# Performance work log

Measured on AMD Instinct MI355X. Metric: run time of the kernel, lower is better.

The kernel has to match this reference:

```python
import jax, jax.numpy as jnp
from jax import lax
import numpy as np

V, E, NF = 50000, 300, 1          # vocab, embed_size, n_features
H = 256                            # hidden size (both layers)
B, TH, TB = 128, 32, 512           # batch, headline len, body len
NC = 4                             # n_classes


def setup_inputs() -> dict:
    key = jax.random.key(0)
    ks = jax.random.split(key, 24)
    emb = jax.random.normal(ks[0], (V, E), jnp.float32) * 0.1
    emb = emb.at[0].set(0.0)  # pad token -> zero row so seqlen masking is meaningful

    def make_ids(kid, klen, T):
        raw = jax.random.randint(kid, (B, T, NF), 1, V)
        lens = jax.random.randint(klen, (B,), max(T // 4, 1), T + 1)
        mask = jnp.arange(T)[None, :, None] < lens[:, None, None]
        return jnp.where(mask, raw, 0)

    headline_ids = make_ids(ks[1], ks[2], TH)
    body_ids = make_ids(ks[3], ks[4], TB)

    def gru_params(k, din, h):
        k1, k2 = jax.random.split(k, 2)
        s = 1.0 / np.sqrt(din + h)
        return (jax.random.normal(k1, (din + h, 2 * h), jnp.float32) * s,
                jnp.ones((2 * h,), jnp.float32),          # TF GRUCell gate bias init = 1.0
                jax.random.normal(k2, (din + h, h), jnp.float32) * s,
                jnp.zeros((h,), jnp.float32))

    D0 = NF * E
    hd0 = gru_params(ks[5], D0, H)
    hd1 = gru_params(ks[6], H, H)
    bd0 = gru_params(ks[7], D0, H)
    bd1 = gru_params(ks[8], H, H)

    W_pred = jax.random.normal(ks[9], (2 * H, NC), jnp.float32) * (1.0 / np.sqrt(2 * H))
    b_pred = jnp.zeros((NC,), jnp.float32)

    out = {"headline_ids": headline_ids, "body_ids": body_ids, "embeddings": emb,
           "W_pred": W_pred, "b_pred": b_pred}
    for pref, p in (("hd0", hd0), ("hd1", hd1), ("bd0", bd0), ("bd1", bd1)):
        out[pref + "_Wg"], out[pref + "_bg"], out[pref + "_Wc"], out[pref + "_bc"] = p
    return out


def _seq_length(x):
    # used = sign(max(|x|, axis=2)); seqlen = sum over time
    return jnp.sum(jnp.sign(jnp.max(jnp.abs(x), axis=2)), axis=1).astype(jnp.int32)


def _gru_layer(x, seqlen, Wg, bg, Wc, bc):
    # x: [B, T, D] -> outputs [B, T, H], final state [B, H]; dynamic_rnn semantics:
    # past seqlen, output is zero and state is copied through.
    Bsz, T, _ = x.shape
    Hh = Wc.shape[1]
    xt = jnp.swapaxes(x, 0, 1)  # [T, B, D]
    tids = jnp.arange(T)

    def step(h, inp):
        xi, t = inp
        xh = jnp.concatenate([xi, h], axis=-1)
        r, u = jnp.split(jax.nn.sigmoid(xh @ Wg + bg), 2, axis=-1)
        c = jnp.tanh(jnp.concatenate([xi, r * h], axis=-1) @ Wc + bc)
        nh = u * h + (1.0 - u) * c
        valid = (t < seqlen)[:, None]
        out = jnp.where(valid, nh, 0.0)
        h_next = jnp.where(valid, nh, h)
        return h_next, out

    h0 = jnp.zeros((Bsz, Hh), x.dtype)
    hf, outs = lax.scan(step, h0, (xt, tids))
    return jnp.swapaxes(outs, 0, 1), hf


def _stream(ids, emb, layers):
    x = emb[ids].reshape(ids.shape[0], ids.shape[1], -1)  # [B, T, NF*E]
    h = None
    for (Wg, bg, Wc, bc) in layers:
        sl = _seq_length(x)  # recomputed from current layer inputs, as in the source
        x, h = _gru_layer(x, sl, Wg, bg, Wc, bc)
    return h


def reference(headline_ids, body_ids, embeddings,
              hd0_Wg, hd0_bg, hd0_Wc, hd0_bc, hd1_Wg, hd1_bg, hd1_Wc, hd1_bc,
              bd0_Wg, bd0_bg, bd0_Wc, bd0_bc, bd1_Wg, bd1_bg, bd1_Wc, bd1_bc,
              W_pred, b_pred):
    h_head = _stream(headline_ids, embeddings,
                     [(hd0_Wg, hd0_bg, hd0_Wc, hd0_bc), (hd1_Wg, hd1_bg, hd1_Wc, hd1_bc)])
    h_body = _stream(body_ids, embeddings,
                     [(bd0_Wg, bd0_bg, bd0_Wc, bd0_bc), (bd1_Wg, bd1_bg, bd1_Wc, bd1_bc)])
    pred_input = jnp.concatenate([h_head, h_body], axis=1)  # [B, 2H]
    return pred_input @ W_pred + b_pred                      # [B, NC]
```

## Files before the change

### kernel.cpp

```cpp
#include <hip/hip_runtime.h>
#include <cstdint>
#include <cstddef>

#define H_    256
#define NG    768
#define BATCH 128
#define TH_   32
#define TB_   512
#define E_    300
#define RPB   16
#define NBLK  (BATCH / RPB)

typedef _Float16 half8 __attribute__((ext_vector_type(8)));
typedef _Float16 half4 __attribute__((ext_vector_type(4)));
typedef float    floatx4 __attribute__((ext_vector_type(4)));

#define AS1 __attribute__((address_space(1)))
#define AS3 __attribute__((address_space(3)))

#define WC_LGKM0 0xC07F
#define WCVM(N)  (0x0F70 | ((N) & 15) | (((N) >> 4) << 14))

__global__ __launch_bounds__(256) void pack_bias(
    const float* __restrict__ bg, const float* __restrict__ bc,
    float* __restrict__ bias)
{
  int idx = blockIdx.x * 256 + threadIdx.x;
  if (idx < NG) bias[idx] = (idx < 2 * H_) ? bg[idx] : bc[idx - 2 * H_];
}

__global__ __launch_bounds__(256) void pack_bx(
    const float* __restrict__ Wg, const float* __restrict__ Wc,
    int din, int KT, _Float16* __restrict__ out)
{
  int idx = blockIdx.x * 256 + threadIdx.x;
  if (idx >= KT * 48 * 64) return;
  int lane = idx & 63, tile = idx >> 6;
  int kt = tile / 48, nt = tile - kt * 48;
  int col = nt * 16 + (lane & 15);
  int k0 = kt * 32 + (lane >> 4) * 8;
  const float* W; int ncols, c2;
  if (col < 2 * H_) { W = Wg; ncols = 2 * H_; c2 = col; }
  else              { W = Wc; ncols = H_;     c2 = col - 2 * H_; }
  _Float16* dst = out + ((size_t)(kt * 48 + nt) * 64 + lane) * 8;
#pragma unroll
  for (int j = 0; j < 8; ++j) {
    int k = k0 + j;
    dst[j] = (k < din) ? (_Float16)W[(size_t)k * ncols + c2] : (_Float16)0.f;
  }
}

__global__ __launch_bounds__(256) void pack_w(
    const float* __restrict__ Wg, const float* __restrict__ Wc, int din,
    _Float16* __restrict__ wpk)
{
  int idx = blockIdx.x * 256 + threadIdx.x;
  if (idx >= 48 * 64) return;
  int tile = idx >> 6, lane = idx & 63;
  int grp = tile >> 4, tt = tile & 15;
  int wv = tt >> 1, s = tt & 1;
  const float* W; int ncols, n0;
  if (grp == 0)      { W = Wg; ncols = 2 * H_; n0 = wv * 32 + s * 16; }
  else if (grp == 1) { W = Wg; ncols = 2 * H_; n0 = 256 + wv * 32 + s * 16; }
  else               { W = Wc; ncols = H_;     n0 = wv * 32 + s * 16; }
  int n = n0 + (lane & 15);
  int kb = (lane >> 4) * 8;
#pragma unroll
  for (int kt = 0; kt < 8; ++kt) {
    _Float16* dst = wpk + ((size_t)(tile * 8 + kt) * 64 + lane) * 8;
#pragma unroll
    for (int j = 0; j < 8; ++j)
      dst[j] = (_Float16)W[(size_t)(din + kt * 32 + kb + j) * ncols + n];
  }
}

__global__ __launch_bounds__(256) void seq_k(const int* __restrict__ ids, int T,
                                             int* __restrict__ seq)
{
  __shared__ int red[256];
  int b = blockIdx.x, tid = threadIdx.x;
  int cnt = 0;
  for (int t = tid; t < T; t += 256) cnt += (ids[b * T + t] != 0) ? 1 : 0;
  red[tid] = cnt;
  __syncthreads();
  for (int s = 128; s > 0; s >>= 1) {
    if (tid < s) red[tid] += red[tid + s];
    __syncthreads();
  }
  if (tid == 0) seq[b] = red[0];
}

struct GruJob {
  const _Float16* G; const _Float16* W; const int* seq;
  _Float16* outp; float* state; int t0; int tc;
};
struct GemmJob {
  const _Float16* Adir; const int* ids; const _Float16* Bpk;
  const float* bias; _Float16* G;
  int K; int KT; int t0; int tcsh; int T;
};
struct StageArgs {
  GruJob  gj[4];
  GemmJob mj[4];
  const float* emb;
  int ngru; int ngemm;
  int goff[4];
};

union SMem {
  struct { _Float16 hpk[4096]; _Float16 rpk[4096]; _Float16 Gs[4][12288]; } g;
  struct { _Float16 Al[2][64 * 40]; _Float16 Bl[2][8 * 512]; } m;
};

__device__ __forceinline__ void gemm_block(const GemmJob& jb, const float* emb,
                                           int lb, SMem& sm)
{
  auto& Al = sm.m.Al;
  auto& Bl = sm.m.Bl;
  const int tid = threadIdx.x;
  const int w = tid >> 6, lane = tid & 63;
  const int quad = lane >> 4, l15 = lane & 15;
  const int gx = lb / 6, gy = lb - gx * 6;
  const int m0 = gx * 64, n0 = gy * 128;
  const int K = jb.K, KT = jb.KT, tcsh = jb.tcsh;
  const int tc = 1 << tcsh;

  const int am = tid >> 3, ak = tid & 7;
  const int arow = m0 + am;
  const _Float16* asrch = nullptr;
  const float*    asrcf = nullptr;
  if (jb.Adir) {
    asrch = jb.Adir + (size_t)arow * K;
  } else {
    int b = arow >> tcsh, tl = arow & (tc - 1);
    asrcf = emb + (size_t)jb.ids[b * jb.T + jb.t0 + tl] * K;
  }

  float a4[4];
  auto loadA = [&](int kt) {
    int k0 = kt * 32 + ak * 4;
    if (asrch) {
      half4 hv = *(const half4*)&asrch[k0];
#pragma unroll
      for (int j = 0; j < 4; ++j) a4[j] = (float)hv[j];
    } else {
#pragma unroll
      for (int j = 0; j < 4; ++j) a4[j] = (k0 + j < K) ? asrcf[k0 + j] : 0.f;
    }
  };
  auto writeA = [&](int buf) {
    half4 v;
#pragma unroll
    for (int j = 0; j < 4; ++j) v[j] = (_Float16)a4[j];
    *(half4*)&Al[buf][am * 40 + ak * 4] = v;
  };
  auto stageB = [&](int kt, int buf) {
    int nt = (n0 >> 4) + w;
    const _Float16* src = jb.Bpk + ((size_t)(kt * 48 + nt) * 64 + lane) * 8;
    __builtin_amdgcn_global_load_lds(
        (const AS1 unsigned int*)src,
        (AS3 unsigned int*)&Bl[buf][w * 512 + lane * 8], 16, 0, 0);
  };

  loadA(0);
  stageB(0, 0);
  writeA(0);
  floatx4 acc[4] = {};

  for (int kt = 0; kt < KT; ++kt) {
    const int buf = kt & 1;
    __syncthreads();
    if (kt + 1 < KT) { loadA(kt + 1); stageB(kt + 1, buf ^ 1); }
    half8 bf = *(const half8*)&Bl[buf][w * 512 + lane * 8];
#pragma unroll
    for (int st = 0; st < 4; ++st) {
      half8 af = *(const half8*)&Al[buf][(st * 16 + l15) * 40 + quad * 8];
      acc[st] = __builtin_amdgcn_mfma_f32_16x16x32_f16(af, bf, acc[st], 0, 0, 0);
    }
    if (kt + 1 < KT) writeA(buf ^ 1);
  }

  int col = n0 + w * 16 + l15;
  float bb = jb.bias[col];
  int g = col >> 8, kk = col & 255;
  int ww = kk >> 5, ss = (kk >> 4) & 1, ll = kk & 15;
  int cc = 2 * g + ss;
#pragma unroll
  for (int st = 0; st < 4; ++st) {
#pragma unroll
    for (int r = 0; r < 4; ++r) {
      int grow = m0 + st * 16 + quad * 4 + r;
      int b = grow >> tcsh, tl = grow & (tc - 1);
      int rg = b >> 4, mm = b & 15, qb = mm >> 2, rb = mm & 3;
      jb.G[((size_t)tl * BATCH + rg * RPB) * NG +
           ((ww * 6 + cc) * 64 + qb * 16 + ll) * 4 + rb] =
          (_Float16)(acc[st][r] + bb);
    }
  }
}

__device__ __forceinline__ void gru_block(const GruJob& jb, int rg, SMem& sm)
{
  _Float16* hpk = sm.g.hpk;
  _Float16* rpk = sm.g.rpk;
  auto& Gs = sm.g.Gs;

  const _Float16* G = jb.G;
  if (!G) return;
  const _Float16* Wsrc = jb.W;
  _Float16* outp = jb.outp;
  float* state = jb.state;
  const int t0 = jb.t0, tc = jb.tc;

  const int tid = threadIdx.x;
  const int w = tid >> 6, lane = tid & 63;
  const int quad = lane >> 4, l15 = lane & 15;

  floatx4 wg[4][8];
  floatx4 wc[2][8];
#pragma unroll
  for (int i = 0; i < 4; ++i) {
    const int tile = (i >> 1) * 16 + w * 2 + (i & 1);
#pragma unroll
    for (int kt = 0; kt < 8; ++kt) {
      wg[i][kt] = *(const floatx4*)&Wsrc[((size_t)(tile * 8 + kt) * 64 + lane) * 8];
      asm volatile("" : "+v"(wg[i][kt]));
    }
  }
#pragma unroll
  for (int i = 0; i < 2; ++i) {
    const int tile = 32 + w * 2 + i;
#pragma unroll
    for (int kt = 0; kt < 8; ++kt) {
      wc[i][kt] = *(const floatx4*)&Wsrc[((size_t)(tile * 8 + kt) * 64 + lane) * 8];
      asm volatile("" : "+a"(wc[i][kt]));
    }
  }

  int seq4[4];
#pragma unroll
  for (int r = 0; r < 4; ++r) seq4[r] = jb.seq[rg * RPB + quad * 4 + r];
  int Smax = 0;
#pragma unroll
  for (int i = 0; i < 16; ++i) Smax = max(Smax, jb.seq[rg * RPB + i]);
  int steps = Smax - t0;
  if (steps < 0) steps = 0;
  if (steps > tc) steps = tc;

  const int wbase = (w * 64 + quad * 2 + (l15 >> 3)) * 8 + (l15 & 7);
  const int rbase = (((quad >> 1) << 5) + ((l15 & 3) << 3) +
                     ((l15 >> 2) << 1) + (quad & 1)) * 8;

  float h_reg[2][4];
#pragma unroll
  for (int s = 0; s < 2; ++s)
#pragma unroll
    for (int r = 0; r < 4; ++r) {
      int row = quad * 4 + r, k = w * 32 + s * 16 + l15;
      float v = (t0 == 0) ? 0.f : state[(size_t)(rg * RPB + row) * H_ + k];
      h_reg[s][r] = v;
      hpk[wbase + s * 256 + r * 64] = (_Float16)v;
    }

  const _Float16* gblk = G + (size_t)rg * RPB * NG + w * 1536;
  _Float16* ldsw = &Gs[0][0] + w * 1536;
  auto stage = [&](int t, int buf) {
    const _Float16* gp = gblk + (size_t)t * BATCH * NG;
    _Float16* lp = ldsw + buf * 12288;
#pragma unroll
    for (int i = 0; i < 3; ++i) {
      __builtin_amdgcn_global_load_lds(
          (const AS1 unsigned int*)(gp + i * 512 + lane * 8),
          (AS3 unsigned int*)(lp + i * 512), 16, 0, 0);
    }
  };
  if (steps > 0) stage(0, 0);
  __syncthreads();
  if (steps > 1) stage(1, 1);
  if (steps > 2) stage(2, 2);

  const _Float16* hA = &hpk[rbase];
  const _Float16* rA = &rpk[rbase];

  __builtin_amdgcn_s_setprio(1);
  for (int t = 0; t < steps; ++t) {
    const int buf = t & 3;
    if (t + 3 < steps) stage(t + 3, (t + 3) & 3);

    floatx4 acc[4] = {};
#pragma unroll
    for (int kt = 0; kt < 8; ++kt) {
      half8 a = *(const half8*)&hA[kt * 512];
#pragma unroll
      for (int s = 0; s < 4; ++s)
        acc[s] = __builtin_amdgcn_mfma_f32_16x16x32_f16(
            a, __builtin_bit_cast(half8, wg[s][kt]), acc[s], 0, 0, 0);
    }

    {
      int np = outp ? ((t < 3) ? t : 3) : 0;
      int nf = steps - 1 - t; if (nf > 3) nf = 3;
      switch (np * 4 + nf) {
        case  0: __builtin_amdgcn_s_waitcnt(WCVM(0));  break;
        case  1: __builtin_amdgcn_s_waitcnt(WCVM(3));  break;
        case  2: __builtin_amdgcn_s_waitcnt(WCVM(6));  break;
        case  3: __builtin_amdgcn_s_waitcnt(WCVM(9));  break;
        case  4: __builtin_amdgcn_s_waitcnt(WCVM(8));  break;
        case  5: __builtin_amdgcn_s_waitcnt(WCVM(11)); break;
        case  6: __builtin_amdgcn_s_waitcnt(WCVM(14)); break;
        case  7: __builtin_amdgcn_s_waitcnt(WCVM(17)); break;
        case  8: __builtin_amdgcn_s_waitcnt(WCVM(16)); break;
        case  9: __builtin_amdgcn_s_waitcnt(WCVM(19)); break;
        case 10: __builtin_amdgcn_s_waitcnt(WCVM(22)); break;
        case 11: __builtin_amdgcn_s_waitcnt(WCVM(25)); break;
        case 12: __builtin_amdgcn_s_waitcnt(WCVM(24)); break;
        case 13: __builtin_amdgcn_s_waitcnt(WCVM(27)); break;
        case 14: __builtin_amdgcn_s_waitcnt(WCVM(30)); break;
        default: __builtin_amdgcn_s_waitcnt(WCVM(33)); break;
      }
    }

    floatx4 gA[4];
#pragma unroll
    for (int c = 0; c < 4; ++c) {
      half4 hv = *(const half4*)&Gs[buf][(w * 6 + c) * 256 + lane * 4];
#pragma unroll
      for (int j = 0; j < 4; ++j) gA[c][j] = (float)hv[j];
    }

#pragma unroll
    for (int s = 0; s < 2; ++s)
#pragma unroll
      for (int r = 0; r < 4; ++r) {
        float pre = acc[s][r] + gA[s][r];
        float g = __builtin_amdgcn_rcpf(1.f + __expf(-pre));
        rpk[wbase + s * 256 + r * 64] = (_Float16)(g * h_reg[s][r]);
      }
    float u_reg[2][4];
#pragma unroll
    for (int s = 0; s < 2; ++s)
#pragma unroll
      for (int r = 0; r < 4; ++r) {
        float pre = acc[2 + s][r] + gA[2 + s][r];
        u_reg[s][r] = __builtin_amdgcn_rcpf(1.f + __expf(-pre));
      }
    __builtin_amdgcn_s_waitcnt(WC_LGKM0);
    __builtin_amdgcn_s_barrier();

    floatx4 accB[2] = {};
#pragma unroll
    for (int kt = 0; kt < 8; ++kt) {
      half8 a = *(const half8*)&rA[kt * 512];
#pragma unroll
      for (int s = 0; s < 2; ++s)
        accB[s] = __builtin_amdgcn_mfma_f32_16x16x32_f16(
            a, __builtin_bit_cast(half8, wc[s][kt]), accB[s], 0, 0, 0);
    }
    floatx4 gB[2];
#pragma unroll
    for (int s = 0; s < 2; ++s) {
      half4 hv = *(const half4*)&Gs[buf][(w * 6 + 4 + s) * 256 + lane * 4];
#pragma unroll
      for (int j = 0; j < 4; ++j) gB[s][j] = (float)hv[j];
    }

#pragma unroll
    for (int s = 0; s < 2; ++s)
#pragma unroll
      for (int r = 0; r < 4; ++r) {
        int row = quad * 4 + r;
        float pre = accB[s][r] + gB[s][r];
        float c = 1.f - 2.f * __builtin_amdgcn_rcpf(1.f + __expf(2.f * pre));
        float u = u_reg[s][r];
        float hn = u * h_reg[s][r] + (1.f - u) * c;
        bool valid = (t0 + t) < seq4[r];
        hn = valid ? hn : h_reg[s][r];
        h_reg[s][r] = hn;
        hpk[wbase + s * 256 + r * 64] = (_Float16)hn;
        if (outp)
          outp[((size_t)(rg * RPB + row) * tc + t) * H_ + (w * 32 + s * 16 + l15)] =
              (_Float16)(valid ? hn : 0.f);
      }
    __builtin_amdgcn_s_waitcnt(WC_LGKM0);
    __builtin_amdgcn_s_barrier();
  }
  __builtin_amdgcn_s_setprio(0);
#pragma unroll
  for (int s = 0; s < 2; ++s)
#pragma unroll
    for (int r = 0; r < 4; ++r)
      state[(size_t)(rg * RPB + quad * 4 + r) * H_ + (w * 32 + s * 16 + l15)] =
          h_reg[s][r];
}

__global__ __launch_bounds__(512, 1) void mega(StageArgs a)
{
  __shared__ SMem sm;
  const int bid = blockIdx.x;
  const int ngrub = a.ngru * NBLK;
  if (bid < ngrub) {
    gru_block(a.gj[bid >> 3], bid & 7, sm);
  } else {
    int lb = bid - ngrub;
    int j = 0;
#pragma unroll
    for (int k = 1; k < 4; ++k)
      if (k < a.ngemm && lb >= a.goff[k]) j = k;
    gemm_block(a.mj[j], a.emb, lb - a.goff[j], sm);
  }
}

__global__ __launch_bounds__(512) void pred_k(
    const float* __restrict__ hh, const float* __restrict__ hb,
    const float* __restrict__ Wp, const float* __restrict__ bpred,
    float* __restrict__ out)
{
  int tid = threadIdx.x;
  int b = tid >> 2, c = tid & 3;
  float acc = bpred[c];
  for (int k = 0; k < H_; ++k) acc += hh[b * H_ + k] * Wp[k * 4 + c];
  for (int k = 0; k < H_; ++k) acc += hb[b * H_ + k] * Wp[(H_ + k) * 4 + c];
  out[b * 4 + c] = acc;
}

extern "C" void kernel_launch(void* const* d_in, const int* in_sizes, int n_in,
                              void* d_out, int out_size, void* d_ws, size_t ws_size,
                              hipStream_t stream)
{
  (void)in_sizes; (void)n_in; (void)out_size;
  const int*   idsH = (const int*)  d_in[0];
  const int*   idsB = (const int*)  d_in[1];
  const float* emb  = (const float*)d_in[2];
  const float* Wp   = (const float*)d_in[3];
  const float* bp   = (const float*)d_in[4];
  const float* W[4][4];
  for (int s = 0; s < 4; ++s)
    for (int q = 0; q < 4; ++q)
      W[s][q] = (const float*)d_in[5 + s * 4 + q];

  float* wbase = (float*)d_ws;
  size_t off = 0;
  auto alloc = [&](size_t n) {
    float* p = wbase + off; off += (n + 255) & ~(size_t)255; return p;
  };
  int* seqH = (int*)alloc(BATCH);
  int* seqB = (int*)alloc(BATCH);
  float* bi[4]; _Float16* Wpk[4]; _Float16* Bxh[4];
  const int din[4] = {E_, H_, E_, H_};
  const int KT[4]  = {10, 8, 10, 8};
  for (int s = 0; s < 4; ++s) {
    bi[s]  = alloc(NG);
    Wpk[s] = (_Float16*)alloc(48 * 8 * 64 * 8 / 2);
    Bxh[s] = (_Float16*)alloc((size_t)KT[s] * 48 * 64 * 8 / 2);
  }
  float* stB0 = alloc((size_t)BATCH * H_);
  float* stH0 = alloc((size_t)BATCH * H_);
  float* hfH  = alloc((size_t)BATCH * H_);
  float* hfB  = alloc((size_t)BATCH * H_);

  const int CHH = 16;
  _Float16* GH0 = (_Float16*)alloc((size_t)BATCH * CHH * NG / 2);
  _Float16* GH1 = (_Float16*)alloc((size_t)BATCH * CHH * NG / 2);
  _Float16* OcH = (_Float16*)alloc((size_t)BATCH * CHH * H_ / 2);

  int CH = 16;
  while (CH > 4 &&
         (off + (size_t)BATCH * CH * (2 * NG + H_) + 2048) * 4 > ws_size)
    CH >>= 1;
  _Float16 *GB0[2], *GB1[2], *OcB[2];
  for (int i = 0; i < 2; ++i) {
    GB0[i] = (_Float16*)alloc((size_t)BATCH * CH * NG / 2);
    GB1[i] = (_Float16*)alloc((size_t)BATCH * CH * NG / 2);
    OcB[i] = (_Float16*)alloc((size_t)BATCH * CH * H_ / 2);
  }
  const int tcshB = __builtin_ctz(CH), tcshH = __builtin_ctz(CHH);
  const int NB = TB_ / CH;

  for (int s = 0; s < 4; ++s) {
    pack_bias<<<(NG + 255) / 256, 256, 0, stream>>>(W[s][1], W[s][3], bi[s]);
    pack_w<<<(48 * 64 + 255) / 256, 256, 0, stream>>>(
        W[s][0], W[s][2], din[s], Wpk[s]);
    pack_bx<<<(KT[s] * 48 * 64 + 255) / 256, 256, 0, stream>>>(
        W[s][0], W[s][2], din[s], KT[s], Bxh[s]);
  }
  seq_k<<<BATCH, 256, 0, stream>>>(idsH, TH_, seqH);
  seq_k<<<BATCH, 256, 0, stream>>>(idsB, TB_, seqB);

  const int nstages = (NB + 3 > 6) ? NB + 3 : 6;
  for (int s = 0; s < nstages; ++s) {
    StageArgs a{};
    a.emb = emb;
    int ng = 0, nm = 0, gacc = 0;
    auto addGru = [&](const _Float16* G, const _Float16* Wk, const int* seq,
                      _Float16* outp, float* st, int t0, int tc) {
      a.gj[ng++] = GruJob{G, Wk, seq, outp, st, t0, tc};
    };
    auto addGemm = [&](const _Float16* Adir, const int* ids, const _Float16* Bpk,
                       const float* bias, _Float16* G, int K, int KTv, int t0,
                       int tcsh, int T, int rows) {
      a.goff[nm] = gacc; gacc += (rows / 64) * 6;
      a.mj[nm++] = GemmJob{Adir, ids, Bpk, bias, G, K, KTv, t0, tcsh, T};
    };

    if (s < NB)
      addGemm(nullptr, idsB, Bxh[2], bi[2], GB0[s & 1], E_, 10, s * CH,
              tcshB, TB_, BATCH * CH);
    if (s >= 1 && s <= NB) {
      int c = s - 1;
      addGru(GB0[c & 1], Wpk[2], seqB, OcB[c & 1], stB0, c * CH, CH);
    }
    if (s >= 2 && s <= NB + 1) {
      int c = s - 2;
      addGemm(OcB[c & 1], nullptr, Bxh[3], bi[3], GB1[c & 1], H_, 8, 0,
              tcshB, TB_, BATCH * CH);
    }
    if (s >= 3 && s <= NB + 2) {
      int c = s - 3;
      addGru(GB1[c & 1], Wpk[3], seqB, nullptr, hfB, c * CH, CH);
    }
    if (s == 0 || s == 2)
      addGemm(nullptr, idsH, Bxh[0], bi[0], GH0, E_, 10, (s >> 1) * CHH,
              tcshH, TH_, BATCH * CHH);
    if (s == 1 || s == 3)
      addGru(GH0, Wpk[0], seqH, OcH, stH0, ((s - 1) >> 1) * CHH, CHH);
    if (s == 2 || s == 4)
      addGemm(OcH, nullptr, Bxh[1], bi[1], GH1, H_, 8, 0, tcshH, TH_,
              BATCH * CHH);
    if (s == 3 || s == 5)
      addGru(GH1, Wpk[1], seqH, nullptr, hfH, ((s - 3) >> 1) * CHH, CHH);

    a.ngru = ng; a.ngemm = nm;
    int nblocks = ng * NBLK + gacc;
    if (nblocks > 0) mega<<<nblocks, 512, 0, stream>>>(a);
  }

  pred_k<<<1, 512, 0, stream>>>(hfH, hfB, Wp, bp, (float*)d_out);
}
```

Baseline: 2.533 ms.

## Replace per-stage kernel launches with one persistent kernel using atomic flag dataflow

Swaps the sequence of ~35 per-stage mega launches for a single persistent kernel. 24 resident GRU blocks keep their recurrent weights in registers across all chunks, and 200 worker blocks pull GEMM tiles from an atomic work queue. Producers and consumers are ordered through per-chunk counters with acquire/release fences, and a 4-slot ring buffer holds intermediate gate inputs. The goal is to remove launch gaps, the state save/reload between stages, and the pipeline bubbles, at the cost of spin-wait overhead and a risk of deadlock if the grid is not fully co-resident.

```diff
diff --git a/kernel.cpp b/kernel.cpp
--- a/kernel.cpp
+++ b/kernel.cpp
@@ -9,7 +9,27 @@
 #define TB_   512
 #define E_    300
 #define RPB   16
-#define NBLK  (BATCH / RPB)
+#define CH_   16
+#define NCH   32
+#define NT_   192
+#define RING  4
+#define NJ    72
+#define NGRU  24
+#define NWORK 200
+#define GRID  (NGRU + NWORK)
+
+#define G0S   ((size_t)BATCH * CH_ * NG)
+#define OCS   ((size_t)BATCH * CH_ * H_)
+
+#define F_QHEAD 0
+#define F_CNT0  1
+#define F_CNT1  33
+#define F_L0F   65
+#define F_L1F   97
+#define F_HCNT0 129
+#define F_HCNT1 131
+#define F_HL0F  133
+#define F_NUM   136
 
 typedef _Float16 half8 __attribute__((ext_vector_type(8)));
 typedef _Float16 half4 __attribute__((ext_vector_type(4)));
@@ -90,26 +110,28 @@
   if (tid == 0) seq[b] = red[0];
 }
 
-struct GruJob {
-  const _Float16* G; const _Float16* W; const int* seq;
-  _Float16* outp; float* state; int t0; int tc;
-};
 struct GemmJob {
   const _Float16* Adir; const int* ids; const _Float16* Bpk;
   const float* bias; _Float16* G;
   int K; int KT; int t0; int tcsh; int T;
 };
-struct StageArgs {
-  GruJob  gj[4];
-  GemmJob mj[4];
-  const float* emb;
-  int ngru; int ngemm;
-  int goff[4];
+
+struct PArgs {
+  const float* emb; const int* idsH; const int* idsB;
+  const int* seqH; const int* seqB;
+  const _Float16 *Wpk0, *Wpk1, *Wpk2, *Wpk3;
+  const _Float16 *Bx0, *Bx1, *Bx2, *Bx3;
+  const float *bi0, *bi1, *bi2, *bi3;
+  _Float16 *G0r, *G1r, *Ocr;
+  _Float16 *GH0, *GH1, *OcH;
+  float *hfH, *hfB;
+  int* flg;
 };
 
 union SMem {
   struct { _Float16 hpk[4096]; _Float16 rpk[4096]; _Float16 Gs[4][12288]; } g;
   struct { _Float16 Al[2][64 * 40]; _Float16 Bl[2][8 * 512]; } m;
+  int bcast;
 };
 
 __device__ __forceinline__ void gemm_block(const GemmJob& jb, const float* emb,
@@ -199,19 +221,22 @@
   }
 }
 
-__device__ __forceinline__ void gru_block(const GruJob& jb, int rg, SMem& sm)
+struct GruRun {
+  const _Float16* W; const int* seq; int rg; int nch;
+  const _Float16* Gb; size_t gs; int ring;
+  _Float16* Ob; size_t os;
+  float* stOut;
+  int* wflag; int wtar;
+  int* w2flag;
+  int* pflag;
+};
+
+__device__ __forceinline__ void gru_run(const GruRun& P, SMem& sm)
 {
   _Float16* hpk = sm.g.hpk;
   _Float16* rpk = sm.g.rpk;
   auto& Gs = sm.g.Gs;
 
-  const _Float16* G = jb.G;
-  if (!G) return;
-  const _Float16* Wsrc = jb.W;
-  _Float16* outp = jb.outp;
-  float* state = jb.state;
-  const int t0 = jb.t0, tc = jb.tc;
-
   const int tid = threadIdx.x;
   const int w = tid >> 6, lane = tid & 63;
   const int quad = lane >> 4, l15 = lane & 15;
@@ -223,7 +248,7 @@
     const int tile = (i >> 1) * 16 + w * 2 + (i & 1);
 #pragma unroll
     for (int kt = 0; kt < 8; ++kt) {
-      wg[i][kt] = *(const floatx4*)&Wsrc[((size_t)(tile * 8 + kt) * 64 + lane) * 8];
+      wg[i][kt] = *(const floatx4*)&P.W[((size_t)(tile * 8 + kt) * 64 + lane) * 8];
       asm volatile("" : "+v"(wg[i][kt]));
     }
   }
@@ -232,20 +257,17 @@
     const int tile = 32 + w * 2 + i;
 #pragma unroll
     for (int kt = 0; kt < 8; ++kt) {
-      wc[i][kt] = *(const floatx4*)&Wsrc[((size_t)(tile * 8 + kt) * 64 + lane) * 8];
+      wc[i][kt] = *(const floatx4*)&P.W[((size_t)(tile * 8 + kt) * 64 + lane) * 8];
       asm volatile("" : "+a"(wc[i][kt]));
     }
   }
 
   int seq4[4];
 #pragma unroll
-  for (int r = 0; r < 4; ++r) seq4[r] = jb.seq[rg * RPB + quad * 4 + r];
+  for (int r = 0; r < 4; ++r) seq4[r] = P.seq[P.rg * RPB + quad * 4 + r];
   int Smax = 0;
 #pragma unroll
-  for (int i = 0; i < 16; ++i) Smax = max(Smax, jb.seq[rg * RPB + i]);
-  int steps = Smax - t0;
-  if (steps < 0) steps = 0;
-  if (steps > tc) steps = tc;
+  for (int i = 0; i < 16; ++i) Smax = max(Smax, P.seq[P.rg * RPB + i]);
 
   const int wbase = (w * 64 + quad * 2 + (l15 >> 3)) * 8 + (l15 & 7);
   const int rbase = (((quad >> 1) << 5) + ((l15 & 3) << 3) +
@@ -256,157 +278,278 @@
   for (int s = 0; s < 2; ++s)
 #pragma unroll
     for (int r = 0; r < 4; ++r) {
-      int row = quad * 4 + r, k = w * 32 + s * 16 + l15;
-      float v = (t0 == 0) ? 0.f : state[(size_t)(rg * RPB + row) * H_ + k];
-      h_reg[s][r] = v;
-      hpk[wbase + s * 256 + r * 64] = (_Float16)v;
-    }
-
-  const _Float16* gblk = G + (size_t)rg * RPB * NG + w * 1536;
-  _Float16* ldsw = &Gs[0][0] + w * 1536;
-  auto stage = [&](int t, int buf) {
-    const _Float16* gp = gblk + (size_t)t * BATCH * NG;
-    _Float16* lp = ldsw + buf * 12288;
-#pragma unroll
-    for (int i = 0; i < 3; ++i) {
-      __builtin_amdgcn_global_load_lds(
-          (const AS1 unsigned int*)(gp + i * 512 + lane * 8),
-          (AS3 unsigned int*)(lp + i * 512), 16, 0, 0);
-    }
-  };
-  if (steps > 0) stage(0, 0);
-  __syncthreads();
-  if (steps > 1) stage(1, 1);
-  if (steps > 2) stage(2, 2);
+      h_reg[s][r] = 0.f;
+      hpk[wbase + s * 256 + r * 64] = (_Float16)0.f;
+    }
 
   const _Float16* hA = &hpk[rbase];
   const _Float16* rA = &rpk[rbase];
 
-  __builtin_amdgcn_s_setprio(1);
-  for (int t = 0; t < steps; ++t) {
-    const int buf = t & 3;
-    if (t + 3 < steps) stage(t + 3, (t + 3) & 3);
-
-    floatx4 acc[4] = {};
-#pragma unroll
-    for (int kt = 0; kt < 8; ++kt) {
-      half8 a = *(const half8*)&hA[kt * 512];
-#pragma unroll
-      for (int s = 0; s < 4; ++s)
-        acc[s] = __builtin_amdgcn_mfma_f32_16x16x32_f16(
-            a, __builtin_bit_cast(half8, wg[s][kt]), acc[s], 0, 0, 0);
-    }
-
-    {
-      int np = outp ? ((t < 3) ? t : 3) : 0;
-      int nf = steps - 1 - t; if (nf > 3) nf = 3;
-      switch (np * 4 + nf) {
-        case  0: __builtin_amdgcn_s_waitcnt(WCVM(0));  break;
-        case  1: __builtin_amdgcn_s_waitcnt(WCVM(3));  break;
-        case  2: __builtin_amdgcn_s_waitcnt(WCVM(6));  break;
-        case  3: __builtin_amdgcn_s_waitcnt(WCVM(9));  break;
-        case  4: __builtin_amdgcn_s_waitcnt(WCVM(8));  break;
-        case  5: __builtin_amdgcn_s_waitcnt(WCVM(11)); break;
-        case  6: __builtin_amdgcn_s_waitcnt(WCVM(14)); break;
-        case  7: __builtin_amdgcn_s_waitcnt(WCVM(17)); break;
-        case  8: __builtin_amdgcn_s_waitcnt(WCVM(16)); break;
-        case  9: __builtin_amdgcn_s_waitcnt(WCVM(19)); break;
-        case 10: __builtin_amdgcn_s_waitcnt(WCVM(22)); break;
-        case 11: __builtin_amdgcn_s_waitcnt(WCVM(25)); break;
-        case 12: __builtin_amdgcn_s_waitcnt(WCVM(24)); break;
-        case 13: __builtin_amdgcn_s_waitcnt(WCVM(27)); break;
-        case 14: __builtin_amdgcn_s_waitcnt(WCVM(30)); break;
-        default: __builtin_amdgcn_s_waitcnt(WCVM(33)); break;
+  for (int c = 0; c < P.nch; ++c) {
+    if (tid == 0) {
+      while (__hip_atomic_load(&P.wflag[c], __ATOMIC_RELAXED,
+                               __HIP_MEMORY_SCOPE_AGENT) < P.wtar)
+        __builtin_amdgcn_s_sleep(2);
+      if (P.w2flag && c >= RING)
+        while (__hip_atomic_load(&P.w2flag[c - RING], __ATOMIC_RELAXED,
+                                 __HIP_MEMORY_SCOPE_AGENT) < NT_)
+          __builtin_amdgcn_s_sleep(2);
+      __builtin_amdgcn_fence(__ATOMIC_ACQUIRE, "agent");
+    }
+    __syncthreads();
+
+    const int slot = P.ring ? (c & (RING - 1)) : c;
+    const _Float16* G = P.Gb + (size_t)slot * P.gs;
+    _Float16* outp = P.Ob ? P.Ob + (size_t)slot * P.os : nullptr;
+    const int t0 = c * CH_;
+    int steps = Smax - t0;
+    if (steps < 0) steps = 0;
+    if (steps > CH_) steps = CH_;
+
+    const _Float16* gblk = G + (size_t)P.rg * RPB * NG + w * 1536;
+    _Float16* ldsw = &Gs[0][0] + w * 1536;
+    auto stage = [&](int t, int buf) {
+      const _Float16* gp = gblk + (size_t)t * BATCH * NG;
+      _Float16* lp = ldsw + buf * 12288;
+#pragma unroll
+      for (int i = 0; i < 3; ++i) {
+        __builtin_amdgcn_global_load_lds(
+            (const AS1 unsigned int*)(gp + i * 512 + lane * 8),
+            (AS3 unsigned int*)(lp + i * 512), 16, 0, 0);
       }
-    }
-
-    floatx4 gA[4];
-#pragma unroll
-    for (int c = 0; c < 4; ++c) {
-      half4 hv = *(const half4*)&Gs[buf][(w * 6 + c) * 256 + lane * 4];
-#pragma unroll
-      for (int j = 0; j < 4; ++j) gA[c][j] = (float)hv[j];
-    }
-
+    };
+    if (steps > 0) stage(0, 0);
+    __syncthreads();
+    if (steps > 1) stage(1, 1);
+    if (steps > 2) stage(2, 2);
+
+    for (int t = 0; t < steps; ++t) {
+      const int buf = t & 3;
+      if (t + 3 < steps) stage(t + 3, (t + 3) & 3);
+
+      floatx4 acc[4] = {};
+#pragma unroll
+      for (int kt = 0; kt < 8; ++kt) {
+        half8 a = *(const half8*)&hA[kt * 512];
+#pragma unroll
+        for (int s = 0; s < 4; ++s)
+          acc[s] = __builtin_amdgcn_mfma_f32_16x16x32_f16(
+              a, __builtin_bit_cast(half8, wg[s][kt]), acc[s], 0, 0, 0);
+      }
+
+      {
+        int np = outp ? ((t < 3) ? t : 3) : 0;
+        int nf = steps - 1 - t; if (nf > 3) nf = 3;
+        switch (np * 4 + nf) {
+          case  0: __builtin_amdgcn_s_waitcnt(WCVM(0));  break;
+          case  1: __builtin_amdgcn_s_waitcnt(WCVM(3));  break;
+          case  2: __builtin_amdgcn_s_waitcnt(WCVM(6));  break;
+          case  3: __builtin_amdgcn_s_waitcnt(WCVM(9));  break;
+          case  4: __builtin_amdgcn_s_waitcnt(WCVM(8));  break;
+          case  5: __builtin_amdgcn_s_waitcnt(WCVM(11)); break;
+          case  6: __builtin_amdgcn_s_waitcnt(WCVM(14)); break;
+          case  7: __builtin_amdgcn_s_waitcnt(WCVM(17)); break;
+          case  8: __builtin_amdgcn_s_waitcnt(WCVM(16)); break;
+          case  9: __builtin_amdgcn_s_waitcnt(WCVM(19)); break;
+          case 10: __builtin_amdgcn_s_waitcnt(WCVM(22)); break;
+          case 11: __builtin_amdgcn_s_waitcnt(WCVM(25)); break;
+          case 12: __builtin_amdgcn_s_waitcnt(WCVM(24)); break;
+          case 13: __builtin_amdgcn_s_waitcnt(WCVM(27)); break;
+          case 14: __builtin_amdgcn_s_waitcnt(WCVM(30)); break;
+          default: __builtin_amdgcn_s_waitcnt(WCVM(33)); break;
+        }
+      }
+
+      floatx4 gA[4];
+#pragma unroll
+      for (int cc = 0; cc < 4; ++cc) {
+        half4 hv = *(const half4*)&Gs[buf][(w * 6 + cc) * 256 + lane * 4];
+#pragma unroll
+        for (int j = 0; j < 4; ++j) gA[cc][j] = (float)hv[j];
+      }
+
+#pragma unroll
+      for (int s = 0; s < 2; ++s)
+#pragma unroll
+        for (int r = 0; r < 4; ++r) {
+          float pre = acc[s][r] + gA[s][r];
+          float g = __builtin_amdgcn_rcpf(1.f + __expf(-pre));
+          rpk[wbase + s * 256 + r * 64] = (_Float16)(g * h_reg[s][r]);
+        }
+      float u_reg[2][4];
+#pragma unroll
+      for (int s = 0; s < 2; ++s)
+#pragma unroll
+        for (int r = 0; r < 4; ++r) {
+          float pre = acc[2 + s][r] + gA[2 + s][r];
+          u_reg[s][r] = __builtin_amdgcn_rcpf(1.f + __expf(-pre));
+        }
+      __builtin_amdgcn_s_waitcnt(WC_LGKM0);
+      __builtin_amdgcn_s_barrier();
+
+      floatx4 accB[2] = {};
+#pragma unroll
+      for (int kt = 0; kt < 8; ++kt) {
+        half8 a = *(const half8*)&rA[kt * 512];
+#pragma unroll
+        for (int s = 0; s < 2; ++s)
+          accB[s] = __builtin_amdgcn_mfma_f32_16x16x32_f16(
+              a, __builtin_bit_cast(half8, wc[s][kt]), accB[s], 0, 0, 0);
+      }
+      floatx4 gB[2];
+#pragma unroll
+      for (int s = 0; s < 2; ++s) {
+        half4 hv = *(const half4*)&Gs[buf][(w * 6 + 4 + s) * 256 + lane * 4];
+#pragma unroll
+        for (int j = 0; j < 4; ++j) gB[s][j] = (float)hv[j];
+      }
+
+#pragma unroll
+      for (int s = 0; s < 2; ++s)
+#pragma unroll
+        for (int r = 0; r < 4; ++r) {
+          int row = quad * 4 + r;
+          float pre = accB[s][r] + gB[s][r];
+          float cv = 1.f - 2.f * __builtin_amdgcn_rcpf(1.f + __expf(2.f * pre));
+          float u = u_reg[s][r];
+          float hn = u * h_reg[s][r] + (1.f - u) * cv;
+          bool valid = (t0 + t) < seq4[r];
+          hn = valid ? hn : h_reg[s][r];
+          h_reg[s][r] = hn;
+          hpk[wbase + s * 256 + r * 64] = (_Float16)hn;
+          if (outp)
+            outp[((size_t)(P.rg * RPB + row) * CH_ + t) * H_ +
+                 (w * 32 + s * 16 + l15)] = (_Float16)(valid ? hn : 0.f);
+        }
+      __builtin_amdgcn_s_waitcnt(WC_LGKM0);
+      __builtin_amdgcn_s_barrier();
+    }
+
+    __syncthreads();
+    if (P.pflag && tid == 0) {
+      __builtin_amdgcn_fence(__ATOMIC_RELEASE, "agent");
+      __hip_atomic_fetch_add(&P.pflag[c], 1, __ATOMIC_RELAXED,
+                             __HIP_MEMORY_SCOPE_AGENT);
+    }
+  }
+
+  if (P.stOut) {
 #pragma unroll
     for (int s = 0; s < 2; ++s)
 #pragma unroll
-      for (int r = 0; r < 4; ++r) {
-        float pre = acc[s][r] + gA[s][r];
-        float g = __builtin_amdgcn_rcpf(1.f + __expf(-pre));
-        rpk[wbase + s * 256 + r * 64] = (_Float16)(g * h_reg[s][r]);
+      for (int r = 0; r < 4; ++r)
+        P.stOut[(size_t)(P.rg * RPB + quad * 4 + r) * H_ +
+                (w * 32 + s * 16 + l15)] = h_reg[s][r];
+  }
+}
+
+__device__ __forceinline__ void worker(const PArgs& a, SMem& sm)
+{
+  int* flg = a.flg;
+  for (;;) {
+    if (threadIdx.x == 0)
+      sm.bcast = __hip_atomic_fetch_add(&flg[F_QHEAD], 1, __ATOMIC_RELAXED,
+                                        __HIP_MEMORY_SCOPE_AGENT);
+    __syncthreads();
+    int tile = sm.bcast;
+    __syncthreads();
+    if (tile >= NJ * NT_) return;
+    int q = tile / NT_, lb = tile - q * NT_;
+
+    GemmJob jb{};
+    int* post = nullptr;
+    int* d1 = nullptr; int d1t = 0;
+    int* d2 = nullptr; int d2t = 0;
+    bool skip = false;
+
+    if (q < 4) {
+      int c = q;
+      jb = {nullptr, a.idsB, a.Bx2, a.bi2, a.G0r + (size_t)(c & 3) * G0S,
+            E_, 10, c * CH_, 4, TB_};
+      post = &flg[F_CNT0 + c];
+    } else if (q < 6) {
+      int c = q - 4;
+      jb = {nullptr, a.idsH, a.Bx0, a.bi0, a.GH0 + (size_t)c * G0S,
+            E_, 10, c * CH_, 4, TH_};
+      post = &flg[F_HCNT0 + c];
+    } else if (q < 8) {
+      int c = q - 6;
+      jb = {a.OcH + (size_t)c * OCS, nullptr, a.Bx1, a.bi1,
+            a.GH1 + (size_t)c * G0S, H_, 8, 0, 4, TH_};
+      d1 = &flg[F_HL0F + c]; d1t = 8;
+      post = &flg[F_HCNT1 + c];
+    } else {
+      int k = (q - 8) >> 1;
+      if (((q - 8) & 1) == 0) {
+        jb = {a.Ocr + (size_t)(k & 3) * OCS, nullptr, a.Bx3, a.bi3,
+              a.G1r + (size_t)(k & 3) * G0S, H_, 8, 0, 4, TB_};
+        d1 = &flg[F_L0F + k]; d1t = 8;
+        if (k >= RING) { d2 = &flg[F_L1F + (k - RING)]; d2t = 8; }
+        post = &flg[F_CNT1 + k];
+      } else {
+        int c = k + 4;
+        if (c >= NCH) skip = true;
+        else {
+          jb = {nullptr, a.idsB, a.Bx2, a.bi2, a.G0r + (size_t)(c & 3) * G0S,
+                E_, 10, c * CH_, 4, TB_};
+          d1 = &flg[F_L0F + (c - RING)]; d1t = 8;
+          post = &flg[F_CNT0 + c];
+        }
       }
-    float u_reg[2][4];
-#pragma unroll
-    for (int s = 0; s < 2; ++s)
-#pragma unroll
-      for (int r = 0; r < 4; ++r) {
-        float pre = acc[2 + s][r] + gA[2 + s][r];
-        u_reg[s][r] = __builtin_amdgcn_rcpf(1.f + __expf(-pre));
-      }
-    __builtin_amdgcn_s_waitcnt(WC_LGKM0);
-    __builtin_amdgcn_s_barrier();
-
-    floatx4 accB[2] = {};
-#pragma unroll
-    for (int kt = 0; kt < 8; ++kt) {
-      half8 a = *(const half8*)&rA[kt * 512];
-#pragma unroll
-      for (int s = 0; s < 2; ++s)
-        accB[s] = __builtin_amdgcn_mfma_f32_16x16x32_f16(
-            a, __builtin_bit_cast(half8, wc[s][kt]), accB[s], 0, 0, 0);
-    }
-    floatx4 gB[2];
-#pragma unroll
-    for (int s = 0; s < 2; ++s) {
-      half4 hv = *(const half4*)&Gs[buf][(w * 6 + 4 + s) * 256 + lane * 4];
-#pragma unroll
-      for (int j = 0; j < 4; ++j) gB[s][j] = (float)hv[j];
-    }
-
-#pragma unroll
-    for (int s = 0; s < 2; ++s)
-#pragma unroll
-      for (int r = 0; r < 4; ++r) {
-        int row = quad * 4 + r;
-        float pre = accB[s][r] + gB[s][r];
-        float c = 1.f - 2.f * __builtin_amdgcn_rcpf(1.f + __expf(2.f * pre));
-        float u = u_reg[s][r];
-        float hn = u * h_reg[s][r] + (1.f - u) * c;
-        bool valid = (t0 + t) < seq4[r];
-        hn = valid ? hn : h_reg[s][r];
-        h_reg[s][r] = hn;
-        hpk[wbase + s * 256 + r * 64] = (_Float16)hn;
-        if (outp)
-          outp[((size_t)(rg * RPB + row) * tc + t) * H_ + (w * 32 + s * 16 + l15)] =
-              (_Float16)(valid ? hn : 0.f);
-      }
-    __builtin_amdgcn_s_waitcnt(WC_LGKM0);
-    __builtin_amdgcn_s_barrier();
-  }
-  __builtin_amdgcn_s_setprio(0);
-#pragma unroll
-  for (int s = 0; s < 2; ++s)
-#pragma unroll
-    for (int r = 0; r < 4; ++r)
-      state[(size_t)(rg * RPB + quad * 4 + r) * H_ + (w * 32 + s * 16 + l15)] =
-          h_reg[s][r];
-}
-
-__global__ __launch_bounds__(512, 1) void mega(StageArgs a)
+    }
+    if (skip) continue;
+
+    if (threadIdx.x == 0) {
+      if (d1)
+        while (__hip_atomic_load(d1, __ATOMIC_RELAXED,
+                                 __HIP_MEMORY_SCOPE_AGENT) < d1t)
+          __builtin_amdgcn_s_sleep(8);
+      if (d2)
+        while (__hip_atomic_load(d2, __ATOMIC_RELAXED,
+                                 __HIP_MEMORY_SCOPE_AGENT) < d2t)
+          __builtin_amdgcn_s_sleep(8);
+      __builtin_amdgcn_fence(__ATOMIC_ACQUIRE, "agent");
+    }
+    __syncthreads();
+
+    gemm_block(jb, a.emb, lb, sm);
+
+    __syncthreads();
+    if (threadIdx.x == 0) {
+      __builtin_amdgcn_fence(__ATOMIC_RELEASE, "agent");
+      __hip_atomic_fetch_add(post, 1, __ATOMIC_RELAXED,
+                             __HIP_MEMORY_SCOPE_AGENT);
+    }
+  }
+}
+
+__global__ __launch_bounds__(512, 1) void pers(PArgs a)
 {
   __shared__ SMem sm;
   const int bid = blockIdx.x;
-  const int ngrub = a.ngru * NBLK;
-  if (bid < ngrub) {
-    gru_block(a.gj[bid >> 3], bid & 7, sm);
+  int* flg = a.flg;
+
+  if (bid < 8) {
+    GruRun P{a.Wpk2, a.seqB, bid, NCH, a.G0r, G0S, 1,
+             a.Ocr, OCS, nullptr,
+             &flg[F_CNT0], NT_, &flg[F_CNT1], &flg[F_L0F]};
+    gru_run(P, sm);
+  } else if (bid < 16) {
+    GruRun P{a.Wpk3, a.seqB, bid - 8, NCH, a.G1r, G0S, 1,
+             nullptr, 0, a.hfB,
+             &flg[F_CNT1], NT_, nullptr, &flg[F_L1F]};
+    gru_run(P, sm);
+  } else if (bid < NGRU) {
+    GruRun P0{a.Wpk0, a.seqH, bid - 16, 2, a.GH0, G0S, 0,
+              a.OcH, OCS, nullptr,
+              &flg[F_HCNT0], NT_, nullptr, &flg[F_HL0F]};
+    gru_run(P0, sm);
+    GruRun P1{a.Wpk1, a.seqH, bid - 16, 2, a.GH1, G0S, 0,
+              nullptr, 0, a.hfH,
+              &flg[F_HCNT1], NT_, nullptr, nullptr};
+    gru_run(P1, sm);
   } else {
-    int lb = bid - ngrub;
-    int j = 0;
-#pragma unroll
-    for (int k = 1; k < 4; ++k)
-      if (k < a.ngemm && lb >= a.goff[k]) j = k;
-    gemm_block(a.mj[j], a.emb, lb - a.goff[j], sm);
+    worker(a, sm);
   }
 }
 
@@ -427,7 +570,7 @@
                               void* d_out, int out_size, void* d_ws, size_t ws_size,
                               hipStream_t stream)
 {
-  (void)in_sizes; (void)n_in; (void)out_size;
+  (void)in_sizes; (void)n_in; (void)out_size; (void)ws_size;
   const int*   idsH = (const int*)  d_in[0];
   const int*   idsB = (const int*)  d_in[1];
   const float* emb  = (const float*)d_in[2];
@@ -443,6 +586,8 @@
   auto alloc = [&](size_t n) {
     float* p = wbase + off; off += (n + 255) & ~(size_t)255; return p;
   };
+
+  int* flg = (int*)alloc(F_NUM);
   int* seqH = (int*)alloc(BATCH);
   int* seqB = (int*)alloc(BATCH);
   float* bi[4]; _Float16* Wpk[4]; _Float16* Bxh[4];
@@ -453,28 +598,17 @@
     Wpk[s] = (_Float16*)alloc(48 * 8 * 64 * 8 / 2);
     Bxh[s] = (_Float16*)alloc((size_t)KT[s] * 48 * 64 * 8 / 2);
   }
-  float* stB0 = alloc((size_t)BATCH * H_);
-  float* stH0 = alloc((size_t)BATCH * H_);
-  float* hfH  = alloc((size_t)BATCH * H_);
-  float* hfB  = alloc((size_t)BATCH * H_);
-
-  const int CHH = 16;
-  _Float16* GH0 = (_Float16*)alloc((size_t)BATCH * CHH * NG / 2);
-  _Float16* GH1 = (_Float16*)alloc((size_t)BATCH * CHH * NG / 2);
-  _Float16* OcH = (_Float16*)alloc((size_t)BATCH * CHH * H_ / 2);
-
-  int CH = 16;
-  while (CH > 4 &&
-         (off + (size_t)BATCH * CH * (2 * NG + H_) + 2048) * 4 > ws_size)
-    CH >>= 1;
-  _Float16 *GB0[2], *GB1[2], *OcB[2];
-  for (int i = 0; i < 2; ++i) {
-    GB0[i] = (_Float16*)alloc((size_t)BATCH * CH * NG / 2);
-    GB1[i] = (_Float16*)alloc((size_t)BATCH * CH * NG / 2);
-    OcB[i] = (_Float16*)alloc((size_t)BATCH * CH * H_ / 2);
-  }
-  const int tcshB = __builtin_ctz(CH), tcshH = __builtin_ctz(CHH);
-  const int NB = TB_ / CH;
+  float* hfH = alloc((size_t)BATCH * H_);
+  float* hfB = alloc((size_t)BATCH * H_);
+
+  _Float16* GH0 = (_Float16*)alloc(2 * G0S / 2);
+  _Float16* GH1 = (_Float16*)alloc(2 * G0S / 2);
+  _Float16* OcH = (_Float16*)alloc(2 * OCS / 2);
+  _Float16* G0r = (_Float16*)alloc(RING * G0S / 2);
+  _Float16* G1r = (_Float16*)alloc(RING * G0S / 2);
+  _Float16* Ocr = (_Float16*)alloc(RING * OCS / 2);
+
+  hipMemsetAsync(flg, 0, F_NUM * sizeof(int), stream);
 
   for (int s = 0; s < 4; ++s) {
     pack_bias<<<(NG + 255) / 256, 256, 0, stream>>>(W[s][1], W[s][3], bi[s]);
@@ -486,53 +620,15 @@
   seq_k<<<BATCH, 256, 0, stream>>>(idsH, TH_, seqH);
   seq_k<<<BATCH, 256, 0, stream>>>(idsB, TB_, seqB);
 
-  const int nstages = (NB + 3 > 6) ? NB + 3 : 6;
-  for (int s = 0; s < nstages; ++s) {
-    StageArgs a{};
-    a.emb = emb;
-    int ng = 0, nm = 0, gacc = 0;
-    auto addGru = [&](const _Float16* G, const _Float16* Wk, const int* seq,
-                      _Float16* outp, float* st, int t0, int tc) {
-      a.gj[ng++] = GruJob{G, Wk, seq, outp, st, t0, tc};
-    };
-    auto addGemm = [&](const _Float16* Adir, const int* ids, const _Float16* Bpk,
-                       const float* bias, _Float16* G, int K, int KTv, int t0,
-                       int tcsh, int T, int rows) {
-      a.goff[nm] = gacc; gacc += (rows / 64) * 6;
-      a.mj[nm++] = GemmJob{Adir, ids, Bpk, bias, G, K, KTv, t0, tcsh, T};
-    };
-
-    if (s < NB)
-      addGemm(nullptr, idsB, Bxh[2], bi[2], GB0[s & 1], E_, 10, s * CH,
-              tcshB, TB_, BATCH * CH);
-    if (s >= 1 && s <= NB) {
-      int c = s - 1;
-      addGru(GB0[c & 1], Wpk[2], seqB, OcB[c & 1], stB0, c * CH, CH);
-    }
-    if (s >= 2 && s <= NB + 1) {
-      int c = s - 2;
-      addGemm(OcB[c & 1], nullptr, Bxh[3], bi[3], GB1[c & 1], H_, 8, 0,
-              tcshB, TB_, BATCH * CH);
-    }
-    if (s >= 3 && s <= NB + 2) {
-      int c = s - 3;
-      addGru(GB1[c & 1], Wpk[3], seqB, nullptr, hfB, c * CH, CH);
-    }
-    if (s == 0 || s == 2)
-      addGemm(nullptr, idsH, Bxh[0], bi[0], GH0, E_, 10, (s >> 1) * CHH,
-              tcshH, TH_, BATCH * CHH);
-    if (s == 1 || s == 3)
-      addGru(GH0, Wpk[0], seqH, OcH, stH0, ((s - 1) >> 1) * CHH, CHH);
-    if (s == 2 || s == 4)
-      addGemm(OcH, nullptr, Bxh[1], bi[1], GH1, H_, 8, 0, tcshH, TH_,
-              BATCH * CHH);
-    if (s == 3 || s == 5)
-      addGru(GH1, Wpk[1], seqH, nullptr, hfH, ((s - 3) >> 1) * CHH, CHH);
-
-    a.ngru = ng; a.ngemm = nm;
-    int nblocks = ng * NBLK + gacc;
-    if (nblocks > 0) mega<<<nblocks, 512, 0, stream>>>(a);
-  }
+  PArgs a;
+  a.emb = emb; a.idsH = idsH; a.idsB = idsB; a.seqH = seqH; a.seqB = seqB;
+  a.Wpk0 = Wpk[0]; a.Wpk1 = Wpk[1]; a.Wpk2 = Wpk[2]; a.Wpk3 = Wpk[3];
+  a.Bx0 = Bxh[0]; a.Bx1 = Bxh[1]; a.Bx2 = Bxh[2]; a.Bx3 = Bxh[3];
+  a.bi0 = bi[0]; a.bi1 = bi[1]; a.bi2 = bi[2]; a.bi3 = bi[3];
+  a.G0r = G0r; a.G1r = G1r; a.Ocr = Ocr;
+  a.GH0 = GH0; a.GH1 = GH1; a.OcH = OcH;
+  a.hfH = hfH; a.hfB = hfB; a.flg = flg;
+  pers<<<GRID, 512, 0, stream>>>(a);
 
   pred_k<<<1, 512, 0, stream>>>(hfH, hfB, Wp, bp, (float*)d_out);
 }
```

New measurement: 2.213 ms. 12.6% less time.
